# Performance work log

Hardware: AMD Instinct MI355X
Metric: run time of the kernel (lower is better)

## Reference

```python
import jax, jax.numpy as jnp
import numpy as np

EPS = 1e-12  # matches torch F.normalize default eps

def _l2norm(v, axis=-1):
    n = jnp.linalg.norm(v, axis=axis, keepdims=True)
    return v / jnp.maximum(n, EPS)

def setup_inputs() -> dict:
    key = jax.random.key(0)
    kx, kk, kv = jax.random.split(key, 3)
    B, C, H, W = 64, 128, 128, 128
    L = 50
    return {
        "x": jax.random.normal(kx, (B, C, H, W), dtype=jnp.float32),
        "keys": jax.random.normal(kk, (L, C), dtype=jnp.float32),
        "values": jax.random.normal(kv, (L, C), dtype=jnp.float32),
    }

def reference(x, keys, values):
    # normality=False path (default)
    b, c, h, w = x.shape
    xt = x.reshape(b, c, h * w).transpose(0, 2, 1)      # [B, N, C]
    nk = _l2norm(keys)                                   # [L, C]
    nx = _l2norm(xt)                                     # [B, N, C]
    cos_sim = jnp.einsum('lc,bnc->bln', nk, nx)          # [B, L, N]
    sim_vec = jax.nn.softmax(cos_sim, axis=1)            # softmax over L slots
    fnorm = jnp.einsum('bln,lc->bnc', sim_vec, values)   # [B, N, C]
    return fnorm.transpose(0, 2, 1).reshape(b, c, h, w)
```

## Files before the change

### kernel.cpp

```cpp
#include <hip/hip_runtime.h>

#define C_DIM 128
#define L_DIM 50
#define LP    52
#define HW    16384
#define LOG2HW 14

__global__ __launch_bounds__(256) void slot_softmax_kernel(
    const float* __restrict__ x,
    const float* __restrict__ keys,
    const float* __restrict__ values,
    float* __restrict__ out)
{
    __shared__ __align__(16) float nkT[C_DIM][LP];
    __shared__ __align__(16) float vT[C_DIM][LP];

    const int tid = threadIdx.x;

    if (tid < L_DIM) {
        float n2 = 0.f;
        #pragma unroll 4
        for (int c = 0; c < C_DIM; ++c) {
            float k = keys[tid * C_DIM + c];
            n2 += k * k;
        }
        float rn = 1.0f / fmaxf(sqrtf(n2), 1e-12f);
        #pragma unroll 4
        for (int c = 0; c < C_DIM; ++c)
            nkT[c][tid] = keys[tid * C_DIM + c] * rn;
    } else if (tid >= 64 && tid < 64 + L_DIM) {
        int l = tid - 64;
        #pragma unroll 4
        for (int c = 0; c < C_DIM; ++c)
            vT[c][l] = values[l * C_DIM + c];
    } else if (tid >= 128 && tid < 130) {
        int l = L_DIM + (tid - 128);
        #pragma unroll 4
        for (int c = 0; c < C_DIM; ++c) {
            nkT[c][l] = 0.f;
            vT[c][l] = 0.f;
        }
    }
    __syncthreads();

    const long long p = (long long)blockIdx.x * 256 + tid;
    const int b = (int)(p >> LOG2HW);
    const int n = (int)(p & (HW - 1));
    const float* xp = x + ((long long)b << (LOG2HW + 7)) + n;
    float*       op = out + ((long long)b << (LOG2HW + 7)) + n;

    float s[LP];
    #pragma unroll
    for (int l = 0; l < LP; ++l) s[l] = 0.f;
    float n2 = 0.f;

    #pragma unroll 2
    for (int c = 0; c < C_DIM; ++c) {
        float xc = xp[(long long)c << LOG2HW];
        n2 += xc * xc;
        const float4* row = (const float4*)&nkT[c][0];
        #pragma unroll
        for (int j = 0; j < LP / 4; ++j) {
            float4 k4 = row[j];
            s[4*j+0] += k4.x * xc;
            s[4*j+1] += k4.y * xc;
            s[4*j+2] += k4.z * xc;
            s[4*j+3] += k4.w * xc;
        }
    }

    float rn = 1.0f / fmaxf(sqrtf(n2), 1e-12f);
    float m = -1e30f;
    #pragma unroll
    for (int l = 0; l < L_DIM; ++l) {
        s[l] *= rn;
        m = fmaxf(m, s[l]);
    }
    float sum = 0.f;
    #pragma unroll
    for (int l = 0; l < L_DIM; ++l) {
        s[l] = __expf(s[l] - m);
        sum += s[l];
    }
    float inv = 1.0f / sum;
    #pragma unroll
    for (int l = 0; l < L_DIM; ++l) s[l] *= inv;
    s[L_DIM] = 0.f;
    s[L_DIM + 1] = 0.f;

    #pragma unroll 2
    for (int c = 0; c < C_DIM; ++c) {
        const float4* row = (const float4*)&vT[c][0];
        float acc = 0.f;
        #pragma unroll
        for (int j = 0; j < LP / 4; ++j) {
            float4 v4 = row[j];
            acc += v4.x * s[4*j+0];
            acc += v4.y * s[4*j+1];
            acc += v4.z * s[4*j+2];
            acc += v4.w * s[4*j+3];
        }
        op[(long long)c << LOG2HW] = acc;
    }
}

extern "C" void kernel_launch(void* const* d_in, const int* in_sizes, int n_in,
                              void* d_out, int out_size, void* d_ws, size_t ws_size,
                              hipStream_t stream) {
    const float* x      = (const float*)d_in[0];
    const float* keys   = (const float*)d_in[1];
    const float* values = (const float*)d_in[2];
    float* out = (float*)d_out;

    const long long pixels = (long long)in_sizes[0] / C_DIM;
    const int blocks = (int)(pixels / 256);

    hipLaunchKernelGGL(slot_softmax_kernel, dim3(blocks), dim3(256), 0, stream,
                       x, keys, values, out);
}
```

Before: 1.254 ms.

## Stream normalized keys and values via scalar loads with two pixels per thread

Adds a one-block prep kernel that writes the normalized, transposed keys and the values into the workspace. The main kernel then reads each channel row with inline-asm s_load_dwordx4 into SGPRs, replacing per-lane LDS float4 reads. Each thread now handles two adjacent pixels using float2 loads and stores. The LDS kernel is kept as a fallback when the workspace is too small. The aim is to remove LDS bandwidth as the bottleneck and reuse each key load across two pixels, at the cost of roughly doubled VGPR pressure (two 50-entry score arrays), an explicit s_waitcnt after every row, and an extra launch.

```diff
diff --git a/kernel.cpp b/kernel.cpp
--- a/kernel.cpp
+++ b/kernel.cpp
@@ -2,103 +2,194 @@
 
 #define C_DIM 128
 #define L_DIM 50
-#define LP    52
+#define ROWP  64
 #define HW    16384
 #define LOG2HW 14
 
-__global__ __launch_bounds__(256) void slot_softmax_kernel(
+typedef float f32x4 __attribute__((ext_vector_type(4)));
+
+__global__ __launch_bounds__(256) void prep_kernel(
+    const float* __restrict__ keys, const float* __restrict__ values,
+    float* __restrict__ ws)
+{
+    __shared__ float rn[L_DIM];
+    const int tid = threadIdx.x;
+    if (tid < L_DIM) {
+        float n2 = 0.f;
+        for (int c = 0; c < C_DIM; ++c) { float k = keys[tid * C_DIM + c]; n2 += k * k; }
+        rn[tid] = 1.0f / fmaxf(sqrtf(n2), 1e-12f);
+    }
+    __syncthreads();
+    if (tid < C_DIM) {
+        const int c = tid;
+        float* nk = ws;
+        float* vv = ws + C_DIM * ROWP;
+        for (int l = 0; l < ROWP; ++l) {
+            nk[c * ROWP + l] = (l < L_DIM) ? keys[l * C_DIM + c] * rn[l] : 0.f;
+            vv[c * ROWP + l] = (l < L_DIM) ? values[l * C_DIM + c] : 0.f;
+        }
+    }
+}
+
+#define SLOAD52(ptr, k0,k1,k2,k3,k4,k5,k6,k7,k8,k9,k10,k11,k12)            \
+    asm("s_load_dwordx4 %0, %13, 0x0\n\t"                                  \
+        "s_load_dwordx4 %1, %13, 0x10\n\t"                                 \
+        "s_load_dwordx4 %2, %13, 0x20\n\t"                                 \
+        "s_load_dwordx4 %3, %13, 0x30\n\t"                                 \
+        "s_load_dwordx4 %4, %13, 0x40\n\t"                                 \
+        "s_load_dwordx4 %5, %13, 0x50\n\t"                                 \
+        "s_load_dwordx4 %6, %13, 0x60\n\t"                                 \
+        "s_load_dwordx4 %7, %13, 0x70\n\t"                                 \
+        "s_load_dwordx4 %8, %13, 0x80\n\t"                                 \
+        "s_load_dwordx4 %9, %13, 0x90\n\t"                                 \
+        "s_load_dwordx4 %10, %13, 0xa0\n\t"                                \
+        "s_load_dwordx4 %11, %13, 0xb0\n\t"                                \
+        "s_load_dwordx4 %12, %13, 0xc0\n\t"                                \
+        "s_waitcnt lgkmcnt(0)"                                             \
+        : "=s"(k0), "=s"(k1), "=s"(k2), "=s"(k3), "=s"(k4), "=s"(k5),      \
+          "=s"(k6), "=s"(k7), "=s"(k8), "=s"(k9), "=s"(k10), "=s"(k11),    \
+          "=s"(k12)                                                        \
+        : "s"(ptr))
+
+#define DOT4(kk, b)                                                        \
+    { s0[b+0] += kk[0] * xv.x;  s1[b+0] += kk[0] * xv.y;                   \
+      s0[b+1] += kk[1] * xv.x;  s1[b+1] += kk[1] * xv.y;                   \
+      s0[b+2] += kk[2] * xv.x;  s1[b+2] += kk[2] * xv.y;                   \
+      s0[b+3] += kk[3] * xv.x;  s1[b+3] += kk[3] * xv.y; }
+
+#define WSUM4(kk, b)                                                       \
+    { acc0 += kk[0] * s0[b+0];  acc1 += kk[0] * s1[b+0];                   \
+      acc0 += kk[1] * s0[b+1];  acc1 += kk[1] * s1[b+1];                   \
+      acc0 += kk[2] * s0[b+2];  acc1 += kk[2] * s1[b+2];                   \
+      acc0 += kk[3] * s0[b+3];  acc1 += kk[3] * s1[b+3]; }
+
+__global__ __launch_bounds__(256) void slot_softmax_scalar(
     const float* __restrict__ x,
-    const float* __restrict__ keys,
-    const float* __restrict__ values,
+    const float* __restrict__ ws,
     float* __restrict__ out)
+{
+    const int tid = threadIdx.x;
+    const long long p0 = ((long long)blockIdx.x * 256 + tid) * 2;
+    const int b = (int)(p0 >> LOG2HW);
+    const int n = (int)(p0 & (HW - 1));
+    const float* xp = x + ((long long)b << (LOG2HW + 7)) + n;
+    float*       op = out + ((long long)b << (LOG2HW + 7)) + n;
+
+    float s0[L_DIM], s1[L_DIM];
+    #pragma unroll
+    for (int l = 0; l < L_DIM; ++l) { s0[l] = 0.f; s1[l] = 0.f; }
+    float n20 = 0.f, n21 = 0.f;
+
+    #pragma unroll 2
+    for (int c = 0; c < C_DIM; ++c) {
+        const float2 xv = *reinterpret_cast<const float2*>(xp + ((long long)c << LOG2HW));
+        const float* kr = ws + c * ROWP;
+        f32x4 k0,k1,k2,k3,k4,k5,k6,k7,k8,k9,k10,k11,k12;
+        SLOAD52(kr, k0,k1,k2,k3,k4,k5,k6,k7,k8,k9,k10,k11,k12);
+        n20 += xv.x * xv.x;
+        n21 += xv.y * xv.y;
+        DOT4(k0, 0)  DOT4(k1, 4)  DOT4(k2, 8)  DOT4(k3, 12)
+        DOT4(k4, 16) DOT4(k5, 20) DOT4(k6, 24) DOT4(k7, 28)
+        DOT4(k8, 32) DOT4(k9, 36) DOT4(k10, 40) DOT4(k11, 44)
+        s0[48] += k12[0] * xv.x;  s1[48] += k12[0] * xv.y;
+        s0[49] += k12[1] * xv.x;  s1[49] += k12[1] * xv.y;
+    }
+
+    const float rn0 = 1.0f / fmaxf(sqrtf(n20), 1e-12f);
+    const float rn1 = 1.0f / fmaxf(sqrtf(n21), 1e-12f);
+    float m0 = -1e30f, m1 = -1e30f;
+    #pragma unroll
+    for (int l = 0; l < L_DIM; ++l) {
+        s0[l] *= rn0;  m0 = fmaxf(m0, s0[l]);
+        s1[l] *= rn1;  m1 = fmaxf(m1, s1[l]);
+    }
+    float sum0 = 0.f, sum1 = 0.f;
+    #pragma unroll
+    for (int l = 0; l < L_DIM; ++l) {
+        s0[l] = __expf(s0[l] - m0);  sum0 += s0[l];
+        s1[l] = __expf(s1[l] - m1);  sum1 += s1[l];
+    }
+    const float inv0 = 1.0f / sum0, inv1 = 1.0f / sum1;
+    #pragma unroll
+    for (int l = 0; l < L_DIM; ++l) { s0[l] *= inv0; s1[l] *= inv1; }
+
+    const float* wsv = ws + C_DIM * ROWP;
+    #pragma unroll 2
+    for (int c = 0; c < C_DIM; ++c) {
+        const float* vr = wsv + c * ROWP;
+        f32x4 k0,k1,k2,k3,k4,k5,k6,k7,k8,k9,k10,k11,k12;
+        SLOAD52(vr, k0,k1,k2,k3,k4,k5,k6,k7,k8,k9,k10,k11,k12);
+        float acc0 = 0.f, acc1 = 0.f;
+        WSUM4(k0, 0)  WSUM4(k1, 4)  WSUM4(k2, 8)  WSUM4(k3, 12)
+        WSUM4(k4, 16) WSUM4(k5, 20) WSUM4(k6, 24) WSUM4(k7, 28)
+        WSUM4(k8, 32) WSUM4(k9, 36) WSUM4(k10, 40) WSUM4(k11, 44)
+        acc0 += k12[0] * s0[48];  acc1 += k12[0] * s1[48];
+        acc0 += k12[1] * s0[49];  acc1 += k12[1] * s1[49];
+        *reinterpret_cast<float2*>(op + ((long long)c << LOG2HW)) = make_float2(acc0, acc1);
+    }
+}
+
+#define LP 52
+__global__ __launch_bounds__(256) void slot_softmax_lds(
+    const float* __restrict__ x, const float* __restrict__ keys,
+    const float* __restrict__ values, float* __restrict__ out)
 {
     __shared__ __align__(16) float nkT[C_DIM][LP];
     __shared__ __align__(16) float vT[C_DIM][LP];
-
     const int tid = threadIdx.x;
-
     if (tid < L_DIM) {
         float n2 = 0.f;
-        #pragma unroll 4
-        for (int c = 0; c < C_DIM; ++c) {
-            float k = keys[tid * C_DIM + c];
-            n2 += k * k;
-        }
-        float rn = 1.0f / fmaxf(sqrtf(n2), 1e-12f);
-        #pragma unroll 4
-        for (int c = 0; c < C_DIM; ++c)
-            nkT[c][tid] = keys[tid * C_DIM + c] * rn;
+        for (int c = 0; c < C_DIM; ++c) { float k = keys[tid*C_DIM+c]; n2 += k*k; }
+        float rnk = 1.0f / fmaxf(sqrtf(n2), 1e-12f);
+        for (int c = 0; c < C_DIM; ++c) nkT[c][tid] = keys[tid*C_DIM+c] * rnk;
     } else if (tid >= 64 && tid < 64 + L_DIM) {
         int l = tid - 64;
-        #pragma unroll 4
-        for (int c = 0; c < C_DIM; ++c)
-            vT[c][l] = values[l * C_DIM + c];
+        for (int c = 0; c < C_DIM; ++c) vT[c][l] = values[l*C_DIM+c];
     } else if (tid >= 128 && tid < 130) {
         int l = L_DIM + (tid - 128);
-        #pragma unroll 4
-        for (int c = 0; c < C_DIM; ++c) {
-            nkT[c][l] = 0.f;
-            vT[c][l] = 0.f;
-        }
+        for (int c = 0; c < C_DIM; ++c) { nkT[c][l] = 0.f; vT[c][l] = 0.f; }
     }
     __syncthreads();
-
     const long long p = (long long)blockIdx.x * 256 + tid;
     const int b = (int)(p >> LOG2HW);
     const int n = (int)(p & (HW - 1));
     const float* xp = x + ((long long)b << (LOG2HW + 7)) + n;
     float*       op = out + ((long long)b << (LOG2HW + 7)) + n;
-
     float s[LP];
     #pragma unroll
     for (int l = 0; l < LP; ++l) s[l] = 0.f;
     float n2 = 0.f;
-
     #pragma unroll 2
     for (int c = 0; c < C_DIM; ++c) {
         float xc = xp[(long long)c << LOG2HW];
         n2 += xc * xc;
         const float4* row = (const float4*)&nkT[c][0];
         #pragma unroll
-        for (int j = 0; j < LP / 4; ++j) {
+        for (int j = 0; j < LP/4; ++j) {
             float4 k4 = row[j];
-            s[4*j+0] += k4.x * xc;
-            s[4*j+1] += k4.y * xc;
-            s[4*j+2] += k4.z * xc;
-            s[4*j+3] += k4.w * xc;
+            s[4*j+0] += k4.x * xc; s[4*j+1] += k4.y * xc;
+            s[4*j+2] += k4.z * xc; s[4*j+3] += k4.w * xc;
         }
     }
-
-    float rn = 1.0f / fmaxf(sqrtf(n2), 1e-12f);
+    float rnx = 1.0f / fmaxf(sqrtf(n2), 1e-12f);
     float m = -1e30f;
     #pragma unroll
-    for (int l = 0; l < L_DIM; ++l) {
-        s[l] *= rn;
-        m = fmaxf(m, s[l]);
-    }
+    for (int l = 0; l < L_DIM; ++l) { s[l] *= rnx; m = fmaxf(m, s[l]); }
     float sum = 0.f;
     #pragma unroll
-    for (int l = 0; l < L_DIM; ++l) {
-        s[l] = __expf(s[l] - m);
-        sum += s[l];
-    }
+    for (int l = 0; l < L_DIM; ++l) { s[l] = __expf(s[l] - m); sum += s[l]; }
     float inv = 1.0f / sum;
     #pragma unroll
     for (int l = 0; l < L_DIM; ++l) s[l] *= inv;
-    s[L_DIM] = 0.f;
-    s[L_DIM + 1] = 0.f;
-
+    s[L_DIM] = 0.f; s[L_DIM+1] = 0.f;
     #pragma unroll 2
     for (int c = 0; c < C_DIM; ++c) {
         const float4* row = (const float4*)&vT[c][0];
         float acc = 0.f;
         #pragma unroll
-        for (int j = 0; j < LP / 4; ++j) {
+        for (int j = 0; j < LP/4; ++j) {
             float4 v4 = row[j];
-            acc += v4.x * s[4*j+0];
-            acc += v4.y * s[4*j+1];
-            acc += v4.z * s[4*j+2];
-            acc += v4.w * s[4*j+3];
+            acc += v4.x*s[4*j+0] + v4.y*s[4*j+1] + v4.z*s[4*j+2] + v4.w*s[4*j+3];
         }
         op[(long long)c << LOG2HW] = acc;
     }
@@ -113,8 +204,17 @@
     float* out = (float*)d_out;
 
     const long long pixels = (long long)in_sizes[0] / C_DIM;
-    const int blocks = (int)(pixels / 256);
-
-    hipLaunchKernelGGL(slot_softmax_kernel, dim3(blocks), dim3(256), 0, stream,
-                       x, keys, values, out);
-}
+
+    if (ws_size >= (size_t)(2 * C_DIM * ROWP * sizeof(float))) {
+        float* ws = (float*)d_ws;
+        hipLaunchKernelGGL(prep_kernel, dim3(1), dim3(256), 0, stream,
+                           keys, values, ws);
+        const int blocks = (int)(pixels / 512);
+        hipLaunchKernelGGL(slot_softmax_scalar, dim3(blocks), dim3(256), 0, stream,
+                           x, ws, out);
+    } else {
+        const int blocks = (int)(pixels / 256);
+        hipLaunchKernelGGL(slot_softmax_lds, dim3(blocks), dim3(256), 0, stream,
+                           x, keys, values, out);
+    }
+}
```

New measurement: 1.190 ms. 5.1% less time.
